# Optimization experiments

Hardware: AMD Instinct MI355X
Metric: run time of the kernel (lower is better)

Reference implementation:

```python
import jax, jax.numpy as jnp
import numpy as np
import math

B, S, D = 2, 2048, 1024
H, DK, DV = 16, 64, 64  # head_count, query_size, value_size; H*DV == D
NEG_INF = -jnp.inf


def setup_inputs() -> dict:
    key = jax.random.key(0)
    ks = jax.random.split(key, 10)
    sc = 0.02
    return {
        "input": jax.random.normal(ks[0], (B, S, D), dtype=jnp.float32),
        "padding_mask": jnp.zeros((B, S), dtype=jnp.float32),  # 0 = valid, 1 = padded
        "wq_w": jax.random.normal(ks[1], (H * DK, D), dtype=jnp.float32) * sc,
        "wq_b": jnp.zeros((H * DK,), dtype=jnp.float32),
        "wk_w": jax.random.normal(ks[2], (H * DK, D), dtype=jnp.float32) * sc,
        "wk_b": jnp.zeros((H * DK,), dtype=jnp.float32),
        "wv_w": jax.random.normal(ks[3], (H * DV, D), dtype=jnp.float32) * sc,
        "wv_b": jnp.zeros((H * DV,), dtype=jnp.float32),
        "fin_w": jax.random.normal(ks[4], (D, H * DV), dtype=jnp.float32) * sc,
        "fin_b": jnp.zeros((D,), dtype=jnp.float32),
    }


def reference(input, padding_mask, wq_w, wq_b, wk_w, wk_b, wv_w, wv_b, fin_w, fin_b):
    b, s, _ = input.shape
    # projections -> [b, h, s, d]
    Q = (input @ wq_w.T + wq_b).reshape(b, s, H, DK).transpose(0, 2, 1, 3)
    K = (input @ wk_w.T + wk_b).reshape(b, s, H, DK).transpose(0, 2, 1, 3)
    V = (input @ wv_w.T + wv_b).reshape(b, s, H, DV).transpose(0, 2, 1, 3)

    # padding mask: pad*(-inf), nan_to_num(0*inf -> 0); broadcast over query dim
    pad = jnp.where(padding_mask > 0, NEG_INF, 0.0)[:, None, None, :]  # [b,1,1,s]
    i = jnp.arange(s)
    causal = jnp.where(i[None, :] < i[:, None] + 1, 0.0, NEG_INF)  # [s,s]
    mask = pad + causal[None, None, :, :]

    # (QK^T + mask) / sqrt(dk), softmax over keys
    logits = (jnp.einsum("bhqd,bhkd->bhqk", Q, K) + mask) / math.sqrt(DK)
    attn = jax.nn.softmax(logits, axis=-1)
    out = jnp.einsum("bhqk,bhkd->bqhd", attn, V).reshape(b, s, H * DV)
    return out @ fin_w.T + fin_b
```

## Files before the change

kernel.cpp:

```cpp
#include <hip/hip_runtime.h>


typedef __bf16 bf16;
typedef __bf16 bf16x4 __attribute__((ext_vector_type(4)));
typedef __bf16 bf16x8 __attribute__((ext_vector_type(8)));
typedef float  f32x4  __attribute__((ext_vector_type(4)));

#define B_  2
#define S_  2048
#define D_  1024
#define H_  16
#define HD  64
#define NEG_BIG (-3.0e38f)
#define SCALE_LOG2E 0.1803368801111204f

__device__ __forceinline__ void lds16(const void* g, void* l) {
    __builtin_amdgcn_global_load_lds((const __attribute__((address_space(1))) void*)g,
                                     (__attribute__((address_space(3))) void*)l, 16, 0, 0);
}

__device__ __forceinline__ f32x4 mfma16(bf16x8 a, bf16x8 b, f32x4 c) {
    return __builtin_amdgcn_mfma_f32_16x16x32_bf16(a, b, c, 0, 0, 0);
}

__global__ __launch_bounds__(256) void convert_k(const float* __restrict__ X,
                                                 const float* __restrict__ wq,
                                                 const float* __restrict__ wk,
                                                 const float* __restrict__ wv,
                                                 const float* __restrict__ wo,
                                                 bf16* __restrict__ dst) {
    const int gid = blockIdx.x * 256 + threadIdx.x;
    const int i   = gid * 4;
    const float* src;
    int off;
    if      (i < (4 << 20)) { src = X;  off = 0; }
    else if (i < (5 << 20)) { src = wq; off = 4 << 20; }
    else if (i < (6 << 20)) { src = wk; off = 5 << 20; }
    else if (i < (7 << 20)) { src = wv; off = 6 << 20; }
    else                    { src = wo; off = 7 << 20; }
    const float4 v = *(const float4*)(src + (i - off));
    bf16x4 p;
    p[0] = (bf16)v.x; p[1] = (bf16)v.y; p[2] = (bf16)v.z; p[3] = (bf16)v.w;
    *(bf16x4*)(dst + i) = p;
}

__global__ __launch_bounds__(256) void gemm_qkv(const bf16* __restrict__ A,
                                                const bf16* __restrict__ Wq,
                                                const bf16* __restrict__ Wk,
                                                const bf16* __restrict__ Wv,
                                                const float* __restrict__ bq,
                                                const float* __restrict__ bk,
                                                const float* __restrict__ bv,
                                                bf16* __restrict__ Qw,
                                                bf16* __restrict__ Kw,
                                                bf16* __restrict__ Vw) {
    constexpr int K = 1024;
    __shared__ bf16 sA[128 * 32];
    __shared__ bf16 sB[128 * 32];
    const int tid  = threadIdx.x;
    const int l15  = tid & 15;
    const int quad = (tid & 63) >> 4;
    const int wid  = tid >> 6;
    const int seg  = blockIdx.x >> 3;
    const int bn   = blockIdx.x & 7;
    const int bm   = blockIdx.y;
    const int wm   = (wid >> 1) * 64;
    const int wn   = (wid & 1) * 64;

    const bf16* W    = (seg == 0) ? Wq : (seg == 1) ? Wk : Wv;
    const float* bias = (seg == 0) ? bq : (seg == 1) ? bk : bv;

    const bf16* Ab = A + (size_t)bm * 128 * K;
    const bf16* Wb = W + (size_t)bn * 128 * K;

    f32x4 acc[4][4] = {};

    for (int k0 = 0; k0 < K; k0 += 32) {
        __syncthreads();
        #pragma unroll
        for (int it = 0; it < 2; ++it) {
            int c = it * 256 + tid;
            int row = c >> 2, c8 = c & 3;
            lds16(Ab + row * K + k0 + c8 * 8, (char*)sA + c * 16);
            lds16(Wb + row * K + k0 + c8 * 8, (char*)sB + c * 16);
        }
        __syncthreads();
        bf16x8 af[4], bfr[4];
        #pragma unroll
        for (int i = 0; i < 4; ++i)
            af[i] = *(const bf16x8*)&sA[(wm + i * 16 + l15) * 32 + quad * 8];
        #pragma unroll
        for (int i = 0; i < 4; ++i)
            bfr[i] = *(const bf16x8*)&sB[(wn + i * 16 + l15) * 32 + quad * 8];
        #pragma unroll
        for (int mi = 0; mi < 4; ++mi)
            #pragma unroll
            for (int ni = 0; ni < 4; ++ni)
                acc[mi][ni] = mfma16(af[mi], bfr[ni], acc[mi][ni]);
    }

    #pragma unroll
    for (int ni = 0; ni < 4; ++ni) {
        const int n  = bn * 128 + wn + ni * 16 + l15;
        const float bv_ = bias[n];
        const int h = n >> 6;
        #pragma unroll
        for (int mi = 0; mi < 4; ++mi) {
            const int m0 = bm * 128 + wm + mi * 16 + quad * 4;
            if (seg == 2) {
                const int dv = n & 63;
                const int b = m0 >> 11, s = m0 & 2047;
                bf16x4 pack;
                #pragma unroll
                for (int r = 0; r < 4; ++r) pack[r] = (bf16)(acc[mi][ni][r] + bv_);
                *(bf16x4*)&Vw[(((size_t)(b * H_ + h) * HD + dv) << 11) + s] = pack;
            } else {
                bf16* C = (seg == 0) ? Qw : Kw;
                const float qs = (seg == 0) ? SCALE_LOG2E : 1.0f;
                const int dk = n & 63;
                #pragma unroll
                for (int r = 0; r < 4; ++r) {
                    const int m = m0 + r, b = m >> 11, s = m & 2047;
                    C[(((size_t)(b * H_ + h) << 11) + s) * HD + dk] =
                        (bf16)((acc[mi][ni][r] + bv_) * qs);
                }
            }
        }
    }
}

__global__ __launch_bounds__(256) void gemm_fin(const bf16* __restrict__ A,
                                                const bf16* __restrict__ W,
                                                const float* __restrict__ bias,
                                                float* __restrict__ C) {
    constexpr int N = 1024, K = 1024;
    __shared__ bf16 sA[64 * 32];
    __shared__ bf16 sB[128 * 32];
    const int tid  = threadIdx.x;
    const int l15  = tid & 15;
    const int quad = (tid & 63) >> 4;
    const int wid  = tid >> 6;
    const int bm   = blockIdx.x >> 3;
    const int bn   = blockIdx.x & 7;
    const int wm   = (wid & 1) * 32;
    const int wn   = (wid >> 1) * 64;

    const bf16* Ab = A + (size_t)bm * 64 * K;
    const bf16* Wb = W + (size_t)bn * 128 * K;

    f32x4 acc[2][4] = {};

    for (int k0 = 0; k0 < K; k0 += 32) {
        __syncthreads();
        {
            int c = tid, row = c >> 2, c8 = c & 3;
            lds16(Ab + row * K + k0 + c8 * 8, (char*)sA + c * 16);
        }
        #pragma unroll
        for (int it = 0; it < 2; ++it) {
            int c = it * 256 + tid;
            int row = c >> 2, c8 = c & 3;
            lds16(Wb + row * K + k0 + c8 * 8, (char*)sB + c * 16);
        }
        __syncthreads();
        bf16x8 af[2], bfr[4];
        #pragma unroll
        for (int i = 0; i < 2; ++i)
            af[i] = *(const bf16x8*)&sA[(wm + i * 16 + l15) * 32 + quad * 8];
        #pragma unroll
        for (int i = 0; i < 4; ++i)
            bfr[i] = *(const bf16x8*)&sB[(wn + i * 16 + l15) * 32 + quad * 8];
        #pragma unroll
        for (int mi = 0; mi < 2; ++mi)
            #pragma unroll
            for (int ni = 0; ni < 4; ++ni)
                acc[mi][ni] = mfma16(af[mi], bfr[ni], acc[mi][ni]);
    }

    #pragma unroll
    for (int ni = 0; ni < 4; ++ni) {
        const int n  = bn * 128 + wn + ni * 16 + l15;
        const float bv = bias[n];
        #pragma unroll
        for (int mi = 0; mi < 2; ++mi) {
            const int m0 = bm * 64 + wm + mi * 16 + quad * 4;
            #pragma unroll
            for (int r = 0; r < 4; ++r)
                C[(size_t)(m0 + r) * N + n] = acc[mi][ni][r] + bv;
        }
    }
}

__global__ __launch_bounds__(256, 2) void attn_k(const bf16* __restrict__ Q,
                                                 const bf16* __restrict__ K,
                                                 const bf16* __restrict__ Vt,
                                                 const float* __restrict__ pmask,
                                                 bf16* __restrict__ Aout) {
    __shared__ bf16 sK_[2 * 128 * 32];
    __shared__ bf16 sV[4 * 64 * 32];
    __shared__ bf16 sP[4096];
    const int tid  = threadIdx.x;
    const int l15  = tid & 15;
    const int quad = (tid & 63) >> 4;
    const int wid  = tid >> 6;
    const int j    = blockIdx.x >> 5;
    const int bh   = blockIdx.x & 31;
    const int b    = bh >> 4;
    const int h    = bh & 15;
    const int a_  = j >> 3, bq_ = j & 7;
    const int qt  = (a_ == 0) ? (31 - bq_) : (a_ == 1) ? bq_
                  : (a_ == 2) ? (23 - bq_) : (8 + bq_);
    const int nkt = (qt >> 1) + 1;

    const bf16* Qg = Q + ((size_t)bh * S_ + qt * 64) * HD;
    #pragma unroll
    for (int it = 0; it < 2; ++it) {
        int c = it * 256 + tid;
        int pl = c >> 8, row = (c >> 2) & 63, c8 = c & 3;
        lds16(Qg + row * HD + pl * 32 + c8 * 8, (char*)sK_ + c * 16);
    }
    const bf16* Kg = K  + (size_t)bh * S_ * HD;
    const bf16* Vg = Vt + (size_t)bh * HD * S_;
    __syncthreads();
    bf16x8 aq[2];
    #pragma unroll
    for (int kk = 0; kk < 2; ++kk)
        aq[kk] = *(const bf16x8*)&sK_[(kk * 64 + wid * 16 + l15) * 32 + quad * 8];

    bf16x8 onesv;
    #pragma unroll
    for (int i = 0; i < 8; ++i) onesv[i] = (bf16)1.0f;

    f32x4 lacc = {};
    f32x4 o[4] = {};
    const int qrow = wid * 16 + quad * 4;
    const int qg0  = qt * 64 + qrow;

    for (int kt = 0; kt < nkt; ++kt) {
        __syncthreads();
        #pragma unroll
        for (int it = 0; it < 4; ++it) {
            int c = it * 256 + tid;
            { int pl = c >> 9, row = (c >> 2) & 127, c8 = c & 3;
              lds16(Kg + (size_t)kt * 128 * HD + row * HD + pl * 32 + c8 * 8,
                    (char*)sK_ + c * 16); }
            { int kc = c >> 8, dv = (c >> 2) & 63, c8 = c & 3;
              lds16(Vg + kt * 128 + dv * S_ + kc * 32 + c8 * 8,
                    (char*)sV + c * 16); }
        }
        __syncthreads();

        f32x4 s[8] = {};
        #pragma unroll
        for (int tc = 0; tc < 8; ++tc)
            #pragma unroll
            for (int kk = 0; kk < 2; ++kk) {
                bf16x8 bk = *(const bf16x8*)
                    &sK_[(kk * 128 + tc * 16 + l15) * 32 + quad * 8];
                s[tc] = mfma16(aq[kk], bk, s[tc]);
            }

        float pmadd[8];
        #pragma unroll
        for (int tc = 0; tc < 8; ++tc) {
            int kg = kt * 128 + tc * 16 + l15;
            pmadd[tc] = (pmask[b * S_ + kg] > 0.f) ? NEG_BIG : 0.f;
        }
        const bool lastt = (kt == nkt - 1);
        #pragma unroll
        for (int tc = 0; tc < 8; ++tc)
            #pragma unroll
            for (int r = 0; r < 4; ++r) {
                float v = s[tc][r] + pmadd[tc];
                if (lastt && (kt * 128 + tc * 16 + l15 > qg0 + r)) v = NEG_BIG;
                s[tc][r] = exp2f(v);
            }

        #pragma unroll
        for (int hf = 0; hf < 2; ++hf) {
            #pragma unroll
            for (int tc4 = 0; tc4 < 4; ++tc4) {
                const int tc   = hf * 4 + tc4;
                const int keyh = tc4 * 16 + l15;
                const int c    = keyh >> 3;
                const int sub  = keyh & 7;
                #pragma unroll
                for (int r = 0; r < 4; ++r) {
                    const int q  = qrow + r;
                    const int cs = c ^ ((q >> 1) & 7);
                    sP[q * 64 + cs * 8 + sub] = (bf16)s[tc][r];
                }
            }
            #pragma unroll
            for (int c2 = 0; c2 < 2; ++c2) {
                const int qr = wid * 16 + l15;
                const int cs = (c2 * 4 + quad) ^ ((qr >> 1) & 7);
                bf16x8 ap = *(const bf16x8*)&sP[qr * 64 + cs * 8];
                const int kc = hf * 2 + c2;
                lacc = mfma16(ap, onesv, lacc);
                #pragma unroll
                for (int vc = 0; vc < 4; ++vc) {
                    bf16x8 bv = *(const bf16x8*)
                        &sV[(kc * 64 + vc * 16 + l15) * 32 + quad * 8];
                    o[vc] = mfma16(ap, bv, o[vc]);
                }
            }
        }
    }

    #pragma unroll
    for (int r = 0; r < 4; ++r) {
        float inv = 1.f / lacc[r];
        size_t base = ((size_t)b * S_ + qg0 + r) * D_ + h * HD;
        #pragma unroll
        for (int vc = 0; vc < 4; ++vc)
            Aout[base + vc * 16 + l15] = (bf16)(o[vc][r] * inv);
    }
}

extern "C" void kernel_launch(void* const* d_in, const int* in_sizes, int n_in,
                              void* d_out, int out_size, void* d_ws, size_t ws_size,
                              hipStream_t stream) {
    const float* X   = (const float*)d_in[0];
    const float* pm  = (const float*)d_in[1];
    const float* wq  = (const float*)d_in[2];
    const float* bq  = (const float*)d_in[3];
    const float* wk  = (const float*)d_in[4];
    const float* bk  = (const float*)d_in[5];
    const float* wv  = (const float*)d_in[6];
    const float* bvb = (const float*)d_in[7];
    const float* wo  = (const float*)d_in[8];
    const float* bo  = (const float*)d_in[9];
    float* out = (float*)d_out;

    char* ws = (char*)d_ws;
    bf16* Xb  = (bf16*)(ws);
    bf16* Wqb = (bf16*)(ws + (8u  << 20));
    bf16* Wkb = (bf16*)(ws + (10u << 20));
    bf16* Wvb = (bf16*)(ws + (12u << 20));
    bf16* Wob = (bf16*)(ws + (14u << 20));
    bf16* Qw  = (bf16*)(ws + (16u << 20));
    bf16* Kw  = (bf16*)(ws + (24u << 20));
    bf16* Vw  = (bf16*)(ws + (32u << 20));
    bf16* Aw  = (bf16*)(ws + (40u << 20));

    convert_k<<<dim3(8192), dim3(256), 0, stream>>>(X, wq, wk, wv, wo, Xb);
    gemm_qkv<<<dim3(24, 32), dim3(256), 0, stream>>>(Xb, Wqb, Wkb, Wvb,
                                                     bq, bk, bvb, Qw, Kw, Vw);
    attn_k<<<dim3(1024), dim3(256), 0, stream>>>(Qw, Kw, Vw, pm, Aw);
    gemm_fin<<<dim3(512), dim3(256), 0, stream>>>(Aw, Wob, bo, out);
}
```

Before: 192.5 us.

## Precompute per-batch padding flags and skip mask loads when unpadded

An extra block in the convert kernel scans the padding mask and writes one any-padded flag per batch. The attention kernel reads that flag and, when a batch has no padding, skips the per-tile global mask loads and uses a plain exp2 path, with the causal check applied only on the last tile. Q is also now stored transposed (dim-major, like V) with vectorized bf16x4 stores, and the attention kernel gathers its Q fragments element by element from LDS. The attention output buffer is moved to alias the X workspace. This adds a small scan, makes the Q fragment reads in LDS scalar and possibly bank-conflicted, and relies on X being dead by the time attention writes its output.

```diff
diff --git a/kernel.cpp b/kernel.cpp
--- a/kernel.cpp
+++ b/kernel.cpp
@@ -28,7 +28,26 @@
                                                  const float* __restrict__ wk,
                                                  const float* __restrict__ wv,
                                                  const float* __restrict__ wo,
-                                                 bf16* __restrict__ dst) {
+                                                 const float* __restrict__ pmask,
+                                                 bf16* __restrict__ dst,
+                                                 int* __restrict__ flags) {
+    if (blockIdx.x == 8192) {
+        __shared__ int f[2];
+        const int t = threadIdx.x;
+        if (t < 2) f[t] = 0;
+        __syncthreads();
+        int any0 = 0, any1 = 0;
+        #pragma unroll
+        for (int i = 0; i < 8; ++i) {
+            any0 |= (pmask[t * 8 + i] > 0.f);
+            any1 |= (pmask[2048 + t * 8 + i] > 0.f);
+        }
+        if (any0) atomicOr(&f[0], 1);
+        if (any1) atomicOr(&f[1], 1);
+        __syncthreads();
+        if (t < 2) flags[t] = f[t];
+        return;
+    }
     const int gid = blockIdx.x * 256 + threadIdx.x;
     const int i   = gid * 4;
     const float* src;
@@ -107,22 +126,23 @@
         #pragma unroll
         for (int mi = 0; mi < 4; ++mi) {
             const int m0 = bm * 128 + wm + mi * 16 + quad * 4;
-            if (seg == 2) {
+            if (seg != 1) {
+                bf16* C = (seg == 0) ? Qw : Vw;
+                const float qs = (seg == 0) ? SCALE_LOG2E : 1.0f;
                 const int dv = n & 63;
                 const int b = m0 >> 11, s = m0 & 2047;
                 bf16x4 pack;
                 #pragma unroll
-                for (int r = 0; r < 4; ++r) pack[r] = (bf16)(acc[mi][ni][r] + bv_);
-                *(bf16x4*)&Vw[(((size_t)(b * H_ + h) * HD + dv) << 11) + s] = pack;
+                for (int r = 0; r < 4; ++r)
+                    pack[r] = (bf16)((acc[mi][ni][r] + bv_) * qs);
+                *(bf16x4*)&C[(((size_t)(b * H_ + h) * HD + dv) << 11) + s] = pack;
             } else {
-                bf16* C = (seg == 0) ? Qw : Kw;
-                const float qs = (seg == 0) ? SCALE_LOG2E : 1.0f;
                 const int dk = n & 63;
                 #pragma unroll
                 for (int r = 0; r < 4; ++r) {
                     const int m = m0 + r, b = m >> 11, s = m & 2047;
-                    C[(((size_t)(b * H_ + h) << 11) + s) * HD + dk] =
-                        (bf16)((acc[mi][ni][r] + bv_) * qs);
+                    Kw[(((size_t)(b * H_ + h) << 11) + s) * HD + dk] =
+                        (bf16)(acc[mi][ni][r] + bv_);
                 }
             }
         }
@@ -195,6 +215,7 @@
                                                  const bf16* __restrict__ K,
                                                  const bf16* __restrict__ Vt,
                                                  const float* __restrict__ pmask,
+                                                 const int* __restrict__ flags,
                                                  bf16* __restrict__ Aout) {
     __shared__ bf16 sK_[2 * 128 * 32];
     __shared__ bf16 sV[4 * 64 * 32];
@@ -211,13 +232,14 @@
     const int qt  = (a_ == 0) ? (31 - bq_) : (a_ == 1) ? bq_
                   : (a_ == 2) ? (23 - bq_) : (8 + bq_);
     const int nkt = (qt >> 1) + 1;
-
-    const bf16* Qg = Q + ((size_t)bh * S_ + qt * 64) * HD;
+    const int padded = flags[b];
+
+    const bf16* Qg = Q + (size_t)bh * HD * S_ + qt * 64;
     #pragma unroll
     for (int it = 0; it < 2; ++it) {
         int c = it * 256 + tid;
-        int pl = c >> 8, row = (c >> 2) & 63, c8 = c & 3;
-        lds16(Qg + row * HD + pl * 32 + c8 * 8, (char*)sK_ + c * 16);
+        int row = c >> 3, c8 = c & 7;
+        lds16(Qg + (size_t)row * S_ + c8 * 8, (char*)sK_ + c * 16);
     }
     const bf16* Kg = K  + (size_t)bh * S_ * HD;
     const bf16* Vg = Vt + (size_t)bh * HD * S_;
@@ -225,7 +247,9 @@
     bf16x8 aq[2];
     #pragma unroll
     for (int kk = 0; kk < 2; ++kk)
-        aq[kk] = *(const bf16x8*)&sK_[(kk * 64 + wid * 16 + l15) * 32 + quad * 8];
+        #pragma unroll
+        for (int jj = 0; jj < 8; ++jj)
+            aq[kk][jj] = sK_[(kk * 32 + quad * 8 + jj) * 64 + wid * 16 + l15];
 
     bf16x8 onesv;
     #pragma unroll
@@ -260,21 +284,40 @@
                 s[tc] = mfma16(aq[kk], bk, s[tc]);
             }
 
-        float pmadd[8];
-        #pragma unroll
-        for (int tc = 0; tc < 8; ++tc) {
-            int kg = kt * 128 + tc * 16 + l15;
-            pmadd[tc] = (pmask[b * S_ + kg] > 0.f) ? NEG_BIG : 0.f;
-        }
         const bool lastt = (kt == nkt - 1);
-        #pragma unroll
-        for (int tc = 0; tc < 8; ++tc)
-            #pragma unroll
-            for (int r = 0; r < 4; ++r) {
-                float v = s[tc][r] + pmadd[tc];
-                if (lastt && (kt * 128 + tc * 16 + l15 > qg0 + r)) v = NEG_BIG;
-                s[tc][r] = exp2f(v);
-            }
+        if (!padded) {
+            if (lastt) {
+                #pragma unroll
+                for (int tc = 0; tc < 8; ++tc)
+                    #pragma unroll
+                    for (int r = 0; r < 4; ++r) {
+                        float v = s[tc][r];
+                        if (kt * 128 + tc * 16 + l15 > qg0 + r) v = NEG_BIG;
+                        s[tc][r] = exp2f(v);
+                    }
+            } else {
+                #pragma unroll
+                for (int tc = 0; tc < 8; ++tc)
+                    #pragma unroll
+                    for (int r = 0; r < 4; ++r)
+                        s[tc][r] = exp2f(s[tc][r]);
+            }
+        } else {
+            float pmadd[8];
+            #pragma unroll
+            for (int tc = 0; tc < 8; ++tc) {
+                int kg = kt * 128 + tc * 16 + l15;
+                pmadd[tc] = (pmask[b * S_ + kg] > 0.f) ? NEG_BIG : 0.f;
+            }
+            #pragma unroll
+            for (int tc = 0; tc < 8; ++tc)
+                #pragma unroll
+                for (int r = 0; r < 4; ++r) {
+                    float v = s[tc][r] + pmadd[tc];
+                    if (lastt && (kt * 128 + tc * 16 + l15 > qg0 + r)) v = NEG_BIG;
+                    s[tc][r] = exp2f(v);
+                }
+        }
 
         #pragma unroll
         for (int hf = 0; hf < 2; ++hf) {
@@ -342,11 +385,12 @@
     bf16* Qw  = (bf16*)(ws + (16u << 20));
     bf16* Kw  = (bf16*)(ws + (24u << 20));
     bf16* Vw  = (bf16*)(ws + (32u << 20));
-    bf16* Aw  = (bf16*)(ws + (40u << 20));
-
-    convert_k<<<dim3(8192), dim3(256), 0, stream>>>(X, wq, wk, wv, wo, Xb);
+    bf16* Aw  = (bf16*)(ws);
+    int*  fl  = (int*)(ws + (40u << 20));
+
+    convert_k<<<dim3(8193), dim3(256), 0, stream>>>(X, wq, wk, wv, wo, pm, Xb, fl);
     gemm_qkv<<<dim3(24, 32), dim3(256), 0, stream>>>(Xb, Wqb, Wkb, Wvb,
                                                      bq, bk, bvb, Qw, Kw, Vw);
-    attn_k<<<dim3(1024), dim3(256), 0, stream>>>(Qw, Kw, Vw, pm, Aw);
+    attn_k<<<dim3(1024), dim3(256), 0, stream>>>(Qw, Kw, Vw, pm, fl, Aw);
     gemm_fin<<<dim3(512), dim3(256), 0, stream>>>(Aw, Wob, bo, out);
 }
```

Result: slower. 204.1 us (+6.0%).
